# Kernel optimization log

Hardware: AMD Instinct MI355X
Metric: run time of the kernel (lower is better)

## Reference

```python
import jax, jax.numpy as jnp
import numpy as np

ALPHA = 0.2        # LeakyReLU negative slope
NEG = -9e15        # mask value used by the torch module
N, FIN, H, D = 4096, 20, 4, 64


def gat_layer(h, adj_mask, W, a_src, a_dst, average):
    """Multi-head GAT layer. W: [H,Fin,Fout], a_src/a_dst: [H,Fout].
    e_ij = LeakyReLU(a_src . Wh_i + a_dst . Wh_j) == a^T [Wh_i || Wh_j],
    identical math to the N x N x 2F concat in the torch code, without
    materializing the pairwise concat tensor."""
    Wh = jnp.einsum('nf,hfo->hno', h, W)                 # [H,N,F]
    f_s = jnp.einsum('hno,ho->hn', Wh, a_src)            # [H,N]
    f_d = jnp.einsum('hno,ho->hn', Wh, a_dst)            # [H,N]
    e = jax.nn.leaky_relu(f_s[:, :, None] + f_d[:, None, :], ALPHA)  # [H,N,N]
    e = jnp.where(adj_mask[None], e, NEG)
    att = jax.nn.softmax(e, axis=-1)
    out = jax.nn.elu(jnp.einsum('hnm,hmo->hno', att, Wh))  # per-head ELU (concat=True inside)
    if average:
        return out.mean(axis=0)                           # [N,F]
    return jnp.transpose(out, (1, 0, 2)).reshape(h.shape[0], -1)  # [N,H*F]


def setup_inputs() -> dict:
    key = jax.random.key(0)
    ks = jax.random.split(key, 6)
    x = jax.random.normal(ks[0], (N, FIN), jnp.float32)
    adj = jax.random.randint(ks[1], (N, N), 0, 2, jnp.int32)
    # layer 0: 20 -> 64 per head, 4 heads, concat -> 256
    W0 = jax.random.normal(ks[2], (H, FIN, D), jnp.float32) * 0.3
    a0 = jax.random.normal(ks[3], (H, 2 * D), jnp.float32) * 0.1
    # layer 1: 256 -> 64 per head, heads averaged
    W1 = jax.random.normal(ks[4], (H, H * D, D), jnp.float32) * 0.06
    a1 = jax.random.normal(ks[5], (H, 2 * D), jnp.float32) * 0.1
    return {"x": x, "adj": adj, "W0": W0, "a0": a0, "W1": W1, "a1": a1}


def reference(x, adj, W0, a0, W1, a1):
    mask = adj > 0
    h = gat_layer(x, mask, W0, a0[:, :D], a0[:, D:], average=False)   # [N, 256]
    return gat_layer(h, mask, W1, a1[:, :D], a1[:, D:], average=True)  # [N, 64]
```

## Files before the change

### kernel.cpp

```cpp
#include <hip/hip_runtime.h>
#include <hip/hip_fp16.h>
#include <math.h>

#define NN 4096
#define FIN 20
#define NH 4
#define DH 64
#define ALPHA 0.2f
#define LOG2E 1.4426950408889634f

typedef _Float16 f16x8 __attribute__((ext_vector_type(8)));
typedef _Float16 f16x4 __attribute__((ext_vector_type(4)));
typedef __fp16 fp16x2 __attribute__((ext_vector_type(2)));
typedef float f32x4 __attribute__((ext_vector_type(4)));

#if defined(__has_builtin)
#if __has_builtin(__builtin_amdgcn_exp2f)
#define FEXP2(x) __builtin_amdgcn_exp2f(x)
#endif
#endif
#ifndef FEXP2
extern "C" __device__ float __ocml_native_exp2_f32(float);
#define FEXP2(x) __ocml_native_exp2_f32(x)
#endif

__device__ inline void gload_lds16(const void* gsrc, void* ldsbase) {
    __builtin_amdgcn_global_load_lds(
        (const __attribute__((address_space(1))) void*)gsrc,
        (__attribute__((address_space(3))) void*)ldsbase, 16, 0, 0);
}

__global__ __launch_bounds__(256) void k_front(const int* __restrict__ adj,
        unsigned char* __restrict__ bits, const float* __restrict__ x,
        const float* __restrict__ W0, const float* __restrict__ a0,
        _Float16* __restrict__ whT, float* __restrict__ fs, float* __restrict__ fd,
        const float* __restrict__ W1, _Float16* __restrict__ w1T) {
    __shared__ float xs[16 * FIN];
    const int bid = blockIdx.x;
    const int tid = threadIdx.x;
    if (bid < 8192) {
        int t = bid * 256 + tid;
        const int4* p = (const int4*)(adj + (size_t)t * 8);
        int4 a = p[0], b = p[1];
        unsigned int byte = 0;
        byte |= (a.x > 0) << 0; byte |= (a.y > 0) << 1;
        byte |= (a.z > 0) << 2; byte |= (a.w > 0) << 3;
        byte |= (b.x > 0) << 4; byte |= (b.y > 0) << 5;
        byte |= (b.z > 0) << 6; byte |= (b.w > 0) << 7;
        bits[t] = (unsigned char)byte;
    } else if (bid < 8448) {
        int n0 = (bid - 8192) * 16;
        for (int i = tid; i < 16 * FIN; i += 256) xs[i] = x[n0 * FIN + i];
        __syncthreads();
        int h = tid >> 6, d = tid & 63;
        float w0r[FIN];
#pragma unroll
        for (int f = 0; f < FIN; ++f) w0r[f] = W0[(h * FIN + f) * DH + d];
        float asrc = a0[h * 2 * DH + d];
        float adst = a0[h * 2 * DH + DH + d];
        f16x8 wv[2];
#pragma unroll
        for (int n = 0; n < 16; ++n) {
            float wh = 0.f;
#pragma unroll
            for (int f = 0; f < FIN; ++f) wh = fmaf(xs[n * FIN + f], w0r[f], wh);
            wv[n >> 3][n & 7] = (_Float16)wh;
            float sv = wh * asrc, dv = wh * adst;
#pragma unroll
            for (int off = 1; off <= 32; off <<= 1) {
                sv += __shfl_xor(sv, off);
                dv += __shfl_xor(dv, off);
            }
            if (d == 0) { fs[h * NN + n0 + n] = sv; fd[h * NN + n0 + n] = dv; }
        }
        _Float16* dst = whT + ((size_t)(h * DH + d) * NN + n0);
        *(f16x8*)(dst) = wv[0];
        *(f16x8*)(dst + 8) = wv[1];
    } else {
        int u = (bid - 8448) * 256 + tid;
        int h = u >> 14, f = (u >> 6) & 255, d = u & 63;
        w1T[((size_t)(h * DH + d) << 8) + f] = (_Float16)W1[u];
    }
}

__global__ __launch_bounds__(512) void k_attn(const float* __restrict__ fs,
        const float* __restrict__ fd, const _Float16* __restrict__ whT,
        const unsigned char* __restrict__ bits,
        float* __restrict__ pv, float* __restrict__ pl) {
    __shared__ __align__(16) char smem[34304];
    const int ch = blockIdx.x & 1;
    const int rowblk = (blockIdx.x >> 1) & 63;
    const int h = blockIdx.x >> 7;
    const int row0 = rowblk << 6;
    const int cb0 = ch << 11;
    const int tid = threadIdx.x;
    const int l = tid & 63, w = tid >> 6;
    const int rl = l & 15, g = l >> 4;
    const int rg = w >> 2, cq = w & 3;
    const int r0 = row0 + rg * 32 + rl;
    const int r1 = r0 + 16;

    float mloc;
    {
        const float4* f4 = (const float4*)(fd + h * NN);
        float4 v0 = f4[tid], v1 = f4[tid + 512];
        mloc = fmaxf(fmaxf(fmaxf(v0.x, v0.y), fmaxf(v0.z, v0.w)),
                     fmaxf(fmaxf(v1.x, v1.y), fmaxf(v1.z, v1.w)));
    }
#pragma unroll
    for (int off = 1; off <= 32; off <<= 1) mloc = fmaxf(mloc, __shfl_xor(mloc, off));
    float* mxs = (float*)(smem + 33792);
    if (l == 0) mxs[w] = mloc;
    __syncthreads();
    const float fm = fmaxf(fmaxf(fmaxf(mxs[0], mxs[1]), fmaxf(mxs[2], mxs[3])),
                           fmaxf(fmaxf(mxs[4], mxs[5]), fmaxf(mxs[6], mxs[7])));

    const float fsr0 = fs[h * NN + r0], fsr1 = fs[h * NN + r1];
    const float su0 = fsr0 + fm, su1 = fsr1 + fm;
    const float m0 = fmaxf(su0, ALPHA * su0);
    const float m1 = fmaxf(su1, ALPHA * su1);
    const float A0 = (fsr0 - m0) * LOG2E, B0 = (ALPHA * fsr0 - m0) * LOG2E;
    const float A1 = (fsr1 - m1) * LOG2E, B1 = (ALPHA * fsr1 - m1) * LOG2E;
    const float* fdp = fd + h * NN + cb0 + cq * 32 + g * 8;
    const unsigned char* bp0 = bits + (size_t)r0 * (NN / 8) + (cb0 >> 3) + cq * 4;
    const unsigned char* bp1 = bits + (size_t)r1 * (NN / 8) + (cb0 >> 3) + cq * 4;
    const _Float16* whb = whT + (size_t)h * DH * NN + cb0;

    const int d0_ = tid >> 4, c0_ = tid & 15;
    const int d1_ = 32 + (tid >> 4), c1_ = tid & 15;
    const _Float16* src0 = whb + (size_t)d0_ * NN + 8 * (c0_ ^ (d0_ & 15));
    const _Float16* src1 = whb + (size_t)d1_ * NN + 8 * (c1_ ^ (d1_ & 15));
    char* dstA0 = smem + w * 1024;
    char* dstA1 = smem + 8192 + w * 1024;
    char* dstB0 = smem + 16384 + w * 1024;
    char* dstB1 = smem + 16384 + 8192 + w * 1024;

    f32x4 acc0[4] = {{0,0,0,0},{0,0,0,0},{0,0,0,0},{0,0,0,0}};
    f32x4 acc1[4] = {{0,0,0,0},{0,0,0,0},{0,0,0,0},{0,0,0,0}};
    f32x4 al0 = {0,0,0,0}, al1 = {0,0,0,0};
    f16x8 ones;
#pragma unroll
    for (int i = 0; i < 8; ++i) ones[i] = (_Float16)1.0f;
    const int rdswz = ((((cq << 2) | g) ^ rl) << 4);

    gload_lds16(src0, dstA0);
    gload_lds16(src1, dstA1);
    float4 faA = *(const float4*)(fdp);
    float4 fbA = *(const float4*)(fdp + 4);
    unsigned int mA0 = *(const unsigned int*)(bp0);
    unsigned int mA1 = *(const unsigned int*)(bp1);
    float4 faB, fbB;
    unsigned int mB0, mB1;
    __syncthreads();

#define COMPUTE(BUF, FA, FB, M0v, M1v)                                          \
    {                                                                           \
        const float fv[8] = {FA.x, FA.y, FA.z, FA.w, FB.x, FB.y, FB.z, FB.w};   \
        f16x8 av0, av1;                                                         \
        const int sh = g << 3;                                                  \
        _Pragma("unroll")                                                       \
        for (int i = 0; i < 8; i += 2) {                                        \
            float ta = fmaxf(fmaf(fv[i], LOG2E, A0), fmaf(fv[i], ALPHA * LOG2E, B0)); \
            ta = ((M0v >> (sh + i)) & 1u) ? ta : -1e30f;                        \
            float tb = fmaxf(fmaf(fv[i+1], LOG2E, A0), fmaf(fv[i+1], ALPHA * LOG2E, B0)); \
            tb = ((M0v >> (sh + i + 1)) & 1u) ? tb : -1e30f;                    \
            fp16x2 p0 = __builtin_amdgcn_cvt_pkrtz(FEXP2(ta), FEXP2(tb));       \
            av0[i] = (_Float16)p0[0]; av0[i+1] = (_Float16)p0[1];               \
            float tc = fmaxf(fmaf(fv[i], LOG2E, A1), fmaf(fv[i], ALPHA * LOG2E, B1)); \
            tc = ((M1v >> (sh + i)) & 1u) ? tc : -1e30f;                        \
            float td = fmaxf(fmaf(fv[i+1], LOG2E, A1), fmaf(fv[i+1], ALPHA * LOG2E, B1)); \
            td = ((M1v >> (sh + i + 1)) & 1u) ? td : -1e30f;                    \
            fp16x2 p1 = __builtin_amdgcn_cvt_pkrtz(FEXP2(tc), FEXP2(td));       \
            av1[i] = (_Float16)p1[0]; av1[i+1] = (_Float16)p1[1];               \
        }                                                                       \
        al0 = __builtin_amdgcn_mfma_f32_16x16x32_f16(av0, ones, al0, 0, 0, 0);  \
        al1 = __builtin_amdgcn_mfma_f32_16x16x32_f16(av1, ones, al1, 0, 0, 0);  \
        _Pragma("unroll")                                                       \
        for (int t4 = 0; t4 < 4; ++t4) {                                        \
            f16x8 bv = *(const f16x8*)((BUF) + ((16 * t4 + rl) << 8) + rdswz);  \
            acc0[t4] = __builtin_amdgcn_mfma_f32_16x16x32_f16(av0, bv, acc0[t4], 0, 0, 0); \
            acc1[t4] = __builtin_amdgcn_mfma_f32_16x16x32_f16(av1, bv, acc1[t4], 0, 0, 0); \
        }                                                                       \
    }

#pragma unroll 1
    for (int k = 0; k < 8; ++k) {
        const int tB = 2 * k + 1;
        gload_lds16(src0 + tB * 128, dstB0);
        gload_lds16(src1 + tB * 128, dstB1);
        faB = *(const float4*)(fdp + tB * 128);
        fbB = *(const float4*)(fdp + tB * 128 + 4);
        mB0 = *(const unsigned int*)(bp0 + tB * 16);
        mB1 = *(const unsigned int*)(bp1 + tB * 16);
        COMPUTE(smem, faA, fbA, mA0, mA1);
        __syncthreads();
        if (k < 7) {
            const int tA = 2 * k + 2;
            gload_lds16(src0 + tA * 128, dstA0);
            gload_lds16(src1 + tA * 128, dstA1);
            faA = *(const float4*)(fdp + tA * 128);
            fbA = *(const float4*)(fdp + tA * 128 + 4);
            mA0 = *(const unsigned int*)(bp0 + tA * 16);
            mA1 = *(const unsigned int*)(bp1 + tA * 16);
        }
        COMPUTE((smem + 16384), faB, fbB, mB0, mB1);
        __syncthreads();
    }
#undef COMPUTE

    float* red = (float*)smem;
    float* lred = (float*)(smem + 33792);
#pragma unroll
    for (int p = 0; p < 2; ++p) {
        if (rg == p) {
#pragma unroll
            for (int t4 = 0; t4 < 4; ++t4)
#pragma unroll
                for (int i = 0; i < 4; ++i) {
                    red[(cq * 32 + 4 * g + i) * 66 + 16 * t4 + rl]      = acc0[t4][i];
                    red[(cq * 32 + 16 + 4 * g + i) * 66 + 16 * t4 + rl] = acc1[t4][i];
                }
            if (rl == 0) {
#pragma unroll
                for (int i = 0; i < 4; ++i) {
                    lred[cq * 32 + 4 * g + i]      = al0[i];
                    lred[cq * 32 + 16 + 4 * g + i] = al1[i];
                }
            }
        }
        __syncthreads();
#pragma unroll
        for (int j = 0; j < 4; ++j) {
            const int R = w * 4 + j;
            float v = 0.f, L = 0.f;
#pragma unroll
            for (int cc = 0; cc < 4; ++cc) {
                v += red[(cc * 32 + R) * 66 + l];
                L += lred[cc * 32 + R];
            }
            const int Rg = row0 + p * 32 + R;
            pv[(((size_t)(ch * NH + h) * NN) + Rg) * 64 + l] = v;
            if (l == 0) pl[(size_t)(ch * NH + h) * NN + Rg] = L;
        }
        __syncthreads();
    }
}

__global__ __launch_bounds__(256) void k_l1wh(const float* __restrict__ pv,
        const float* __restrict__ pl, const _Float16* __restrict__ w1T,
        const float* __restrict__ a1, float* __restrict__ fs, float* __restrict__ fd) {
    __shared__ float red[4][16][64];
    __shared__ _Float16 lt[16][64];
    int h = blockIdx.x >> 8;
    int row0 = (blockIdx.x & 255) << 4;
    int tid = threadIdx.x;
    int l = tid & 63, w = tid >> 6;
    int rl = l & 15, g = l >> 4;
    const int row = row0 + rl;
    const float L2 = pl[(size_t)w * NN + row] + pl[(size_t)(NH + w) * NN + row];
    const float rcpL = __builtin_amdgcn_rcpf(L2);
    const float* p0 = pv + (((size_t)w * NN) + row) * 64;
    const float* p1 = pv + (((size_t)(NH + w) * NN) + row) * 64;
    f32x4 acc[4] = {{0,0,0,0},{0,0,0,0},{0,0,0,0},{0,0,0,0}};
    const _Float16* bp = w1T + ((size_t)h * DH << 8) + w * 64;
#pragma unroll
    for (int j = 0; j < 2; ++j) {
        int fb = j * 32 + 8 * g;
        float4 va = *(const float4*)(p0 + fb);
        float4 vb = *(const float4*)(p0 + fb + 4);
        float4 wa = *(const float4*)(p1 + fb);
        float4 wb = *(const float4*)(p1 + fb + 4);
        float o[8] = {va.x + wa.x, va.y + wa.y, va.z + wa.z, va.w + wa.w,
                      vb.x + wb.x, vb.y + wb.y, vb.z + wb.z, vb.w + wb.w};
        f16x8 avv;
#pragma unroll
        for (int i = 0; i < 8; ++i) {
            float v = o[i] * rcpL;
            v = v > 0.f ? v : __expf(v) - 1.f;
            avv[i] = (_Float16)v;
        }
#pragma unroll
        for (int t4 = 0; t4 < 4; ++t4) {
            f16x8 bv = *(const f16x8*)(bp + ((size_t)(16 * t4 + rl) << 8) + j * 32 + 8 * g);
            acc[t4] = __builtin_amdgcn_mfma_f32_16x16x32_f16(avv, bv, acc[t4], 0, 0, 0);
        }
    }
#pragma unroll
    for (int t4 = 0; t4 < 4; ++t4)
#pragma unroll
        for (int i = 0; i < 4; ++i) red[w][t4 * 4 + i][l] = acc[t4][i];
    __syncthreads();
#pragma unroll
    for (int i = 0; i < 4; ++i) {
        float v = red[0][w * 4 + i][l] + red[1][w * 4 + i][l]
                + red[2][w * 4 + i][l] + red[3][w * 4 + i][l];
        lt[4 * g + i][16 * w + rl] = (_Float16)v;
    }
    __syncthreads();
    int d = tid & 63, rb = tid >> 6;
    float as_ = a1[h * 2 * DH + d], ad_ = a1[h * 2 * DH + DH + d];
    float svj[4], dvj[4];
#pragma unroll
    for (int j = 0; j < 4; ++j) {
        float wv = (float)lt[rb * 4 + j][d];
        svj[j] = wv * as_;
        dvj[j] = wv * ad_;
    }
#pragma unroll
    for (int off = 1; off <= 32; off <<= 1) {
#pragma unroll
        for (int j = 0; j < 4; ++j) {
            svj[j] += __shfl_xor(svj[j], off);
            dvj[j] += __shfl_xor(dvj[j], off);
        }
    }
    if (d == 0) {
#pragma unroll
        for (int j = 0; j < 4; ++j) {
            fs[h * NN + row0 + rb * 4 + j] = svj[j];
            fd[h * NN + row0 + rb * 4 + j] = dvj[j];
        }
    }
    f16x4 o;
#pragma unroll
    for (int j = 0; j < 4; ++j) o[j] = lt[rb * 4 + j][d];
    _Float16* whT = (_Float16*)nullptr;
    (void)whT;
}

__global__ __launch_bounds__(256) void k_l1whB(const float* __restrict__ pv,
        const float* __restrict__ pl, const _Float16* __restrict__ w1T,
        const float* __restrict__ a1, _Float16* __restrict__ whT,
        float* __restrict__ fs, float* __restrict__ fd) {
    __shared__ float red[4][16][64];
    __shared__ _Float16 lt[16][64];
    int h = blockIdx.x >> 8;
    int row0 = (blockIdx.x & 255) << 4;
    int tid = threadIdx.x;
    int l = tid & 63, w = tid >> 6;
    int rl = l & 15, g = l >> 4;
    const int row = row0 + rl;
    const float L2 = pl[(size_t)w * NN + row] + pl[(size_t)(NH + w) * NN + row];
    const float rcpL = __builtin_amdgcn_rcpf(L2);
    const float* p0 = pv + (((size_t)w * NN) + row) * 64;
    const float* p1 = pv + (((size_t)(NH + w) * NN) + row) * 64;
    f32x4 acc[4] = {{0,0,0,0},{0,0,0,0},{0,0,0,0},{0,0,0,0}};
    const _Float16* bp = w1T + ((size_t)h * DH << 8) + w * 64;
#pragma unroll
    for (int j = 0; j < 2; ++j) {
        int fb = j * 32 + 8 * g;
        float4 va = *(const float4*)(p0 + fb);
        float4 vb = *(const float4*)(p0 + fb + 4);
        float4 wa = *(const float4*)(p1 + fb);
        float4 wb = *(const float4*)(p1 + fb + 4);
        float o[8] = {va.x + wa.x, va.y + wa.y, va.z + wa.z, va.w + wa.w,
                      vb.x + wb.x, vb.y + wb.y, vb.z + wb.z, vb.w + wb.w};
        f16x8 avv;
#pragma unroll
        for (int i = 0; i < 8; ++i) {
            float v = o[i] * rcpL;
            v = v > 0.f ? v : __expf(v) - 1.f;
            avv[i] = (_Float16)v;
        }
#pragma unroll
        for (int t4 = 0; t4 < 4; ++t4) {
            f16x8 bv = *(const f16x8*)(bp + ((size_t)(16 * t4 + rl) << 8) + fb);
            acc[t4] = __builtin_amdgcn_mfma_f32_16x16x32_f16(avv, bv, acc[t4], 0, 0, 0);
        }
    }
#pragma unroll
    for (int t4 = 0; t4 < 4; ++t4)
#pragma unroll
        for (int i = 0; i < 4; ++i) red[w][t4 * 4 + i][l] = acc[t4][i];
    __syncthreads();
#pragma unroll
    for (int i = 0; i < 4; ++i) {
        float v = red[0][w * 4 + i][l] + red[1][w * 4 + i][l]
                + red[2][w * 4 + i][l] + red[3][w * 4 + i][l];
        lt[4 * g + i][16 * w + rl] = (_Float16)v;
    }
    __syncthreads();
    int d = tid & 63, rb = tid >> 6;
    f16x4 o;
#pragma unroll
    for (int j = 0; j < 4; ++j) o[j] = lt[rb * 4 + j][d];
    *(f16x4*)(whT + (size_t)(h * DH + d) * NN + row0 + rb * 4) = o;
    float as_ = a1[h * 2 * DH + d], ad_ = a1[h * 2 * DH + DH + d];
    float svj[4], dvj[4];
#pragma unroll
    for (int j = 0; j < 4; ++j) {
        float wv = (float)lt[rb * 4 + j][d];
        svj[j] = wv * as_;
        dvj[j] = wv * ad_;
    }
#pragma unroll
    for (int off = 1; off <= 32; off <<= 1) {
#pragma unroll
        for (int j = 0; j < 4; ++j) {
            svj[j] += __shfl_xor(svj[j], off);
            dvj[j] += __shfl_xor(dvj[j], off);
        }
    }
    if (d == 0) {
#pragma unroll
        for (int j = 0; j < 4; ++j) {
            fs[h * NN + row0 + rb * 4 + j] = svj[j];
            fd[h * NN + row0 + rb * 4 + j] = dvj[j];
        }
    }
}

__global__ __launch_bounds__(256) void k_merge1(const float* __restrict__ pv,
        const float* __restrict__ pl, float* __restrict__ out) {
    int t = blockIdx.x * 256 + threadIdx.x;
    int d = t & 63, n = t >> 6;
    float s = 0.f;
#pragma unroll
    for (int h = 0; h < NH; ++h) {
        float v = pv[(((size_t)h * NN) + n) * 64 + d] + pv[(((size_t)(NH + h) * NN) + n) * 64 + d];
        float L = pl[(size_t)h * NN + n] + pl[(size_t)(NH + h) * NN + n];
        float o = v * __builtin_amdgcn_rcpf(L);
        s += o > 0.f ? o : __expf(o) - 1.f;
    }
    out[t] = 0.25f * s;
}

extern "C" void kernel_launch(void* const* d_in, const int* in_sizes, int n_in,
                              void* d_out, int out_size, void* d_ws, size_t ws_size,
                              hipStream_t stream) {
    const float* x  = (const float*)d_in[0];
    const int* adj  = (const int*)d_in[1];
    const float* W0 = (const float*)d_in[2];
    const float* a0 = (const float*)d_in[3];
    const float* W1 = (const float*)d_in[4];
    const float* a1 = (const float*)d_in[5];
    float* out = (float*)d_out;
    char* ws = (char*)d_ws;

    unsigned char* bits = (unsigned char*)(ws);
    _Float16* whT0 = (_Float16*)(ws + (2ull << 20));
    _Float16* w1T  = (_Float16*)(ws + (6ull << 20));
    _Float16* whT1 = (_Float16*)(ws + (6ull << 20) + (256ull << 10));
    float* fs0  = (float*)(ws + (9ull << 20));
    float* fd0  = fs0 + NH * NN;
    float* fs1  = fd0 + NH * NN;
    float* fd1  = fs1 + NH * NN;
    float* pv   = (float*)(ws + (10ull << 20));
    float* pl   = (float*)(ws + (18ull << 20));

    k_front<<<8704, 256, 0, stream>>>(adj, bits, x, W0, a0, whT0, fs0, fd0, W1, w1T);
    k_attn<<<2 * NH * (NN / 64), 512, 0, stream>>>(fs0, fd0, whT0, bits, pv, pl);
    k_l1whB<<<NH * (NN / 16), 256, 0, stream>>>(pv, pl, w1T, a1, whT1, fs1, fd1);
    k_attn<<<2 * NH * (NN / 64), 512, 0, stream>>>(fs1, fd1, whT1, bits, pv, pl);
    k_merge1<<<(NN * DH) / 256, 256, 0, stream>>>(pv, pl, out);
}
```

Baseline: 111.4 us.

## Double attention block width to 16 waves with 256-column tiles

Raises k_attn from 512 to 1024 threads so each block runs 8 column-slice waves per row group instead of 4. Each pipeline stage now stages 256 columns of Wh into LDS, which doubles the shared buffers, and the loop trip count halves. The final cross-wave reduction now sums 8 partials. The aim is fewer loop iterations and barriers per column, paid for with higher LDS use per block, possibly lower occupancy and a costlier reduction. A dead kernel is also removed and its replacement renamed.

```diff
diff --git a/kernel.cpp b/kernel.cpp
--- a/kernel.cpp
+++ b/kernel.cpp
@@ -83,11 +83,11 @@
     }
 }
 
-__global__ __launch_bounds__(512) void k_attn(const float* __restrict__ fs,
+__global__ __launch_bounds__(1024) void k_attn(const float* __restrict__ fs,
         const float* __restrict__ fd, const _Float16* __restrict__ whT,
         const unsigned char* __restrict__ bits,
         float* __restrict__ pv, float* __restrict__ pl) {
-    __shared__ __align__(16) char smem[34304];
+    __shared__ __align__(16) char smem[69632];
     const int ch = blockIdx.x & 1;
     const int rowblk = (blockIdx.x >> 1) & 63;
     const int h = blockIdx.x >> 7;
@@ -96,24 +96,23 @@
     const int tid = threadIdx.x;
     const int l = tid & 63, w = tid >> 6;
     const int rl = l & 15, g = l >> 4;
-    const int rg = w >> 2, cq = w & 3;
+    const int rg = w >> 3, cs = w & 7;
     const int r0 = row0 + rg * 32 + rl;
     const int r1 = r0 + 16;
 
     float mloc;
     {
-        const float4* f4 = (const float4*)(fd + h * NN);
-        float4 v0 = f4[tid], v1 = f4[tid + 512];
-        mloc = fmaxf(fmaxf(fmaxf(v0.x, v0.y), fmaxf(v0.z, v0.w)),
-                     fmaxf(fmaxf(v1.x, v1.y), fmaxf(v1.z, v1.w)));
+        float4 v0 = ((const float4*)(fd + h * NN))[tid];
+        mloc = fmaxf(fmaxf(v0.x, v0.y), fmaxf(v0.z, v0.w));
     }
 #pragma unroll
     for (int off = 1; off <= 32; off <<= 1) mloc = fmaxf(mloc, __shfl_xor(mloc, off));
-    float* mxs = (float*)(smem + 33792);
+    float* mxs = (float*)(smem + 67584);
     if (l == 0) mxs[w] = mloc;
     __syncthreads();
-    const float fm = fmaxf(fmaxf(fmaxf(mxs[0], mxs[1]), fmaxf(mxs[2], mxs[3])),
-                           fmaxf(fmaxf(mxs[4], mxs[5]), fmaxf(mxs[6], mxs[7])));
+    float fm = mxs[0];
+#pragma unroll
+    for (int i = 1; i < 16; ++i) fm = fmaxf(fm, mxs[i]);
 
     const float fsr0 = fs[h * NN + r0], fsr1 = fs[h * NN + r1];
     const float su0 = fsr0 + fm, su1 = fsr1 + fm;
@@ -121,19 +120,19 @@
     const float m1 = fmaxf(su1, ALPHA * su1);
     const float A0 = (fsr0 - m0) * LOG2E, B0 = (ALPHA * fsr0 - m0) * LOG2E;
     const float A1 = (fsr1 - m1) * LOG2E, B1 = (ALPHA * fsr1 - m1) * LOG2E;
-    const float* fdp = fd + h * NN + cb0 + cq * 32 + g * 8;
-    const unsigned char* bp0 = bits + (size_t)r0 * (NN / 8) + (cb0 >> 3) + cq * 4;
-    const unsigned char* bp1 = bits + (size_t)r1 * (NN / 8) + (cb0 >> 3) + cq * 4;
+    const float* fdp = fd + h * NN + cb0 + cs * 32 + g * 8;
+    const unsigned char* bp0 = bits + (size_t)r0 * (NN / 8) + (cb0 >> 3) + cs * 4;
+    const unsigned char* bp1 = bits + (size_t)r1 * (NN / 8) + (cb0 >> 3) + cs * 4;
     const _Float16* whb = whT + (size_t)h * DH * NN + cb0;
 
-    const int d0_ = tid >> 4, c0_ = tid & 15;
-    const int d1_ = 32 + (tid >> 4), c1_ = tid & 15;
-    const _Float16* src0 = whb + (size_t)d0_ * NN + 8 * (c0_ ^ (d0_ & 15));
-    const _Float16* src1 = whb + (size_t)d1_ * NN + 8 * (c1_ ^ (d1_ & 15));
+    const int pd = tid >> 5, ps = tid & 31;
+    const int d0_ = pd, d1_ = 32 + pd;
+    const _Float16* src0 = whb + (size_t)d0_ * NN + 8 * (ps ^ (d0_ & 15));
+    const _Float16* src1 = whb + (size_t)d1_ * NN + 8 * (ps ^ (d1_ & 15));
     char* dstA0 = smem + w * 1024;
-    char* dstA1 = smem + 8192 + w * 1024;
-    char* dstB0 = smem + 16384 + w * 1024;
-    char* dstB1 = smem + 16384 + 8192 + w * 1024;
+    char* dstA1 = smem + 16384 + w * 1024;
+    char* dstB0 = smem + 32768 + w * 1024;
+    char* dstB1 = smem + 32768 + 16384 + w * 1024;
 
     f32x4 acc0[4] = {{0,0,0,0},{0,0,0,0},{0,0,0,0},{0,0,0,0}};
     f32x4 acc1[4] = {{0,0,0,0},{0,0,0,0},{0,0,0,0},{0,0,0,0}};
@@ -141,7 +140,7 @@
     f16x8 ones;
 #pragma unroll
     for (int i = 0; i < 8; ++i) ones[i] = (_Float16)1.0f;
-    const int rdswz = ((((cq << 2) | g) ^ rl) << 4);
+    const int rdswz = ((((cs << 2) | g) ^ rl) << 4);
 
     gload_lds16(src0, dstA0);
     gload_lds16(src1, dstA1);
@@ -177,39 +176,39 @@
         al1 = __builtin_amdgcn_mfma_f32_16x16x32_f16(av1, ones, al1, 0, 0, 0);  \
         _Pragma("unroll")                                                       \
         for (int t4 = 0; t4 < 4; ++t4) {                                        \
-            f16x8 bv = *(const f16x8*)((BUF) + ((16 * t4 + rl) << 8) + rdswz);  \
+            f16x8 bv = *(const f16x8*)((BUF) + ((16 * t4 + rl) << 9) + rdswz);  \
             acc0[t4] = __builtin_amdgcn_mfma_f32_16x16x32_f16(av0, bv, acc0[t4], 0, 0, 0); \
             acc1[t4] = __builtin_amdgcn_mfma_f32_16x16x32_f16(av1, bv, acc1[t4], 0, 0, 0); \
         }                                                                       \
     }
 
 #pragma unroll 1
-    for (int k = 0; k < 8; ++k) {
+    for (int k = 0; k < 4; ++k) {
         const int tB = 2 * k + 1;
-        gload_lds16(src0 + tB * 128, dstB0);
-        gload_lds16(src1 + tB * 128, dstB1);
-        faB = *(const float4*)(fdp + tB * 128);
-        fbB = *(const float4*)(fdp + tB * 128 + 4);
-        mB0 = *(const unsigned int*)(bp0 + tB * 16);
-        mB1 = *(const unsigned int*)(bp1 + tB * 16);
+        gload_lds16(src0 + tB * 256, dstB0);
+        gload_lds16(src1 + tB * 256, dstB1);
+        faB = *(const float4*)(fdp + tB * 256);
+        fbB = *(const float4*)(fdp + tB * 256 + 4);
+        mB0 = *(const unsigned int*)(bp0 + tB * 32);
+        mB1 = *(const unsigned int*)(bp1 + tB * 32);
         COMPUTE(smem, faA, fbA, mA0, mA1);
         __syncthreads();
-        if (k < 7) {
+        if (k < 3) {
             const int tA = 2 * k + 2;
-            gload_lds16(src0 + tA * 128, dstA0);
-            gload_lds16(src1 + tA * 128, dstA1);
-            faA = *(const float4*)(fdp + tA * 128);
-            fbA = *(const float4*)(fdp + tA * 128 + 4);
-            mA0 = *(const unsigned int*)(bp0 + tA * 16);
-            mA1 = *(const unsigned int*)(bp1 + tA * 16);
-        }
-        COMPUTE((smem + 16384), faB, fbB, mB0, mB1);
+            gload_lds16(src0 + tA * 256, dstA0);
+            gload_lds16(src1 + tA * 256, dstA1);
+            faA = *(const float4*)(fdp + tA * 256);
+            fbA = *(const float4*)(fdp + tA * 256 + 4);
+            mA0 = *(const unsigned int*)(bp0 + tA * 32);
+            mA1 = *(const unsigned int*)(bp1 + tA * 32);
+        }
+        COMPUTE((smem + 32768), faB, fbB, mB0, mB1);
         __syncthreads();
     }
 #undef COMPUTE
 
     float* red = (float*)smem;
-    float* lred = (float*)(smem + 33792);
+    float* lred = (float*)(smem + 67584);
 #pragma unroll
     for (int p = 0; p < 2; ++p) {
         if (rg == p) {
@@ -217,24 +216,24 @@
             for (int t4 = 0; t4 < 4; ++t4)
 #pragma unroll
                 for (int i = 0; i < 4; ++i) {
-                    red[(cq * 32 + 4 * g + i) * 66 + 16 * t4 + rl]      = acc0[t4][i];
-                    red[(cq * 32 + 16 + 4 * g + i) * 66 + 16 * t4 + rl] = acc1[t4][i];
+                    red[(cs * 32 + 4 * g + i) * 66 + 16 * t4 + rl]      = acc0[t4][i];
+                    red[(cs * 32 + 16 + 4 * g + i) * 66 + 16 * t4 + rl] = acc1[t4][i];
                 }
             if (rl == 0) {
 #pragma unroll
                 for (int i = 0; i < 4; ++i) {
-                    lred[cq * 32 + 4 * g + i]      = al0[i];
-                    lred[cq * 32 + 16 + 4 * g + i] = al1[i];
+                    lred[cs * 32 + 4 * g + i]      = al0[i];
+                    lred[cs * 32 + 16 + 4 * g + i] = al1[i];
                 }
             }
         }
         __syncthreads();
 #pragma unroll
-        for (int j = 0; j < 4; ++j) {
-            const int R = w * 4 + j;
+        for (int j = 0; j < 2; ++j) {
+            const int R = w * 2 + j;
             float v = 0.f, L = 0.f;
 #pragma unroll
-            for (int cc = 0; cc < 4; ++cc) {
+            for (int cc = 0; cc < 8; ++cc) {
                 v += red[(cc * 32 + R) * 66 + l];
                 L += lred[cc * 32 + R];
             }
@@ -247,88 +246,6 @@
 }
 
 __global__ __launch_bounds__(256) void k_l1wh(const float* __restrict__ pv,
-        const float* __restrict__ pl, const _Float16* __restrict__ w1T,
-        const float* __restrict__ a1, float* __restrict__ fs, float* __restrict__ fd) {
-    __shared__ float red[4][16][64];
-    __shared__ _Float16 lt[16][64];
-    int h = blockIdx.x >> 8;
-    int row0 = (blockIdx.x & 255) << 4;
-    int tid = threadIdx.x;
-    int l = tid & 63, w = tid >> 6;
-    int rl = l & 15, g = l >> 4;
-    const int row = row0 + rl;
-    const float L2 = pl[(size_t)w * NN + row] + pl[(size_t)(NH + w) * NN + row];
-    const float rcpL = __builtin_amdgcn_rcpf(L2);
-    const float* p0 = pv + (((size_t)w * NN) + row) * 64;
-    const float* p1 = pv + (((size_t)(NH + w) * NN) + row) * 64;
-    f32x4 acc[4] = {{0,0,0,0},{0,0,0,0},{0,0,0,0},{0,0,0,0}};
-    const _Float16* bp = w1T + ((size_t)h * DH << 8) + w * 64;
-#pragma unroll
-    for (int j = 0; j < 2; ++j) {
-        int fb = j * 32 + 8 * g;
-        float4 va = *(const float4*)(p0 + fb);
-        float4 vb = *(const float4*)(p0 + fb + 4);
-        float4 wa = *(const float4*)(p1 + fb);
-        float4 wb = *(const float4*)(p1 + fb + 4);
-        float o[8] = {va.x + wa.x, va.y + wa.y, va.z + wa.z, va.w + wa.w,
-                      vb.x + wb.x, vb.y + wb.y, vb.z + wb.z, vb.w + wb.w};
-        f16x8 avv;
-#pragma unroll
-        for (int i = 0; i < 8; ++i) {
-            float v = o[i] * rcpL;
-            v = v > 0.f ? v : __expf(v) - 1.f;
-            avv[i] = (_Float16)v;
-        }
-#pragma unroll
-        for (int t4 = 0; t4 < 4; ++t4) {
-            f16x8 bv = *(const f16x8*)(bp + ((size_t)(16 * t4 + rl) << 8) + j * 32 + 8 * g);
-            acc[t4] = __builtin_amdgcn_mfma_f32_16x16x32_f16(avv, bv, acc[t4], 0, 0, 0);
-        }
-    }
-#pragma unroll
-    for (int t4 = 0; t4 < 4; ++t4)
-#pragma unroll
-        for (int i = 0; i < 4; ++i) red[w][t4 * 4 + i][l] = acc[t4][i];
-    __syncthreads();
-#pragma unroll
-    for (int i = 0; i < 4; ++i) {
-        float v = red[0][w * 4 + i][l] + red[1][w * 4 + i][l]
-                + red[2][w * 4 + i][l] + red[3][w * 4 + i][l];
-        lt[4 * g + i][16 * w + rl] = (_Float16)v;
-    }
-    __syncthreads();
-    int d = tid & 63, rb = tid >> 6;
-    float as_ = a1[h * 2 * DH + d], ad_ = a1[h * 2 * DH + DH + d];
-    float svj[4], dvj[4];
-#pragma unroll
-    for (int j = 0; j < 4; ++j) {
-        float wv = (float)lt[rb * 4 + j][d];
-        svj[j] = wv * as_;
-        dvj[j] = wv * ad_;
-    }
-#pragma unroll
-    for (int off = 1; off <= 32; off <<= 1) {
-#pragma unroll
-        for (int j = 0; j < 4; ++j) {
-            svj[j] += __shfl_xor(svj[j], off);
-            dvj[j] += __shfl_xor(dvj[j], off);
-        }
-    }
-    if (d == 0) {
-#pragma unroll
-        for (int j = 0; j < 4; ++j) {
-            fs[h * NN + row0 + rb * 4 + j] = svj[j];
-            fd[h * NN + row0 + rb * 4 + j] = dvj[j];
-        }
-    }
-    f16x4 o;
-#pragma unroll
-    for (int j = 0; j < 4; ++j) o[j] = lt[rb * 4 + j][d];
-    _Float16* whT = (_Float16*)nullptr;
-    (void)whT;
-}
-
-__global__ __launch_bounds__(256) void k_l1whB(const float* __restrict__ pv,
         const float* __restrict__ pl, const _Float16* __restrict__ w1T,
         const float* __restrict__ a1, _Float16* __restrict__ whT,
         float* __restrict__ fs, float* __restrict__ fd) {
@@ -449,8 +366,8 @@
     float* pl   = (float*)(ws + (18ull << 20));
 
     k_front<<<8704, 256, 0, stream>>>(adj, bits, x, W0, a0, whT0, fs0, fd0, W1, w1T);
-    k_attn<<<2 * NH * (NN / 64), 512, 0, stream>>>(fs0, fd0, whT0, bits, pv, pl);
-    k_l1whB<<<NH * (NN / 16), 256, 0, stream>>>(pv, pl, w1T, a1, whT1, fs1, fd1);
-    k_attn<<<2 * NH * (NN / 64), 512, 0, stream>>>(fs1, fd1, whT1, bits, pv, pl);
+    k_attn<<<2 * NH * (NN / 64), 1024, 0, stream>>>(fs0, fd0, whT0, bits, pv, pl);
+    k_l1wh<<<NH * (NN / 16), 256, 0, stream>>>(pv, pl, w1T, a1, whT1, fs1, fd1);
+    k_attn<<<2 * NH * (NN / 64), 1024, 0, stream>>>(fs1, fd1, whT1, bits, pv, pl);
     k_merge1<<<(NN * DH) / 256, 256, 0, stream>>>(pv, pl, out);
 }
```

New measurement: 128.9 us. +15.7%, slower.
